# Performance work log

Measured on AMD Instinct MI355X. Metric: run time of the kernel, lower is better.

## Reference

```python
import jax, jax.numpy as jnp
import numpy as np

B, C, CI = 4, 1024, 512
T, H, W = 16, 28, 28
STD = 0.01  # init std used by the torch module
BN_EPS = 1e-5


def _conv1x1(x, w, b):
    # x: (B,C,T,H,W), w: (O,C), b: (O,)
    return jnp.einsum('bcthw,oc->bothw', x, w) + b[None, :, None, None, None]


def _maxpool2(x):
    # 3D max pool, kernel=stride=2 over (T,H,W)
    b, c, t, h, w = x.shape
    x = x.reshape(b, c, t // 2, 2, h // 2, 2, w // 2, 2)
    return x.max(axis=(3, 5, 7))


def setup_inputs() -> dict:
    key = jax.random.key(0)
    ks = jax.random.split(key, 6)
    return {
        'x': jax.random.normal(ks[0], (B, C, T, H, W), jnp.float32),
        'g_w': STD * jax.random.normal(ks[1], (CI, C), jnp.float32),
        'g_b': jnp.zeros((CI,), jnp.float32),
        'theta_w': STD * jax.random.normal(ks[2], (CI, C), jnp.float32),
        'theta_b': jnp.zeros((CI,), jnp.float32),
        'phi_w': STD * jax.random.normal(ks[3], (CI, C), jnp.float32),
        'phi_b': jnp.zeros((CI,), jnp.float32),
        'w_w': STD * jax.random.normal(ks[4], (C, CI), jnp.float32),
        'w_b': jnp.zeros((C,), jnp.float32),
        'bn_gamma': STD * jax.random.normal(ks[5], (C,), jnp.float32),
        'bn_beta': jnp.zeros((C,), jnp.float32),
    }


def reference(x, g_w, g_b, theta_w, theta_b, phi_w, phi_b, w_w, w_b, bn_gamma, bn_beta):
    b = x.shape[0]
    # g and phi branches are sub-sampled by maxpool(2)
    g_x = _maxpool2(_conv1x1(x, g_w, g_b)).reshape(b, CI, -1)          # (B,Ci,M)
    g_x = g_x.transpose(0, 2, 1)                                        # (B,M,Ci)
    theta_x = _conv1x1(x, theta_w, theta_b).reshape(b, CI, -1)          # (B,Ci,N)
    theta_x = theta_x.transpose(0, 2, 1)                                # (B,N,Ci)
    phi_x = _maxpool2(_conv1x1(x, phi_w, phi_b)).reshape(b, CI, -1)     # (B,Ci,M)
    # embedded gaussian: softmax(theta @ phi) @ g  (unscaled)
    f = jnp.einsum('bnc,bcm->bnm', theta_x, phi_x)                      # (B,N,M)
    f_div_C = jax.nn.softmax(f, axis=-1)
    y = jnp.einsum('bnm,bmc->bnc', f_div_C, g_x)                        # (B,N,Ci)
    y = y.transpose(0, 2, 1).reshape(b, CI, *x.shape[2:])               # (B,Ci,T,H,W)
    # W: 1x1 conv + BatchNorm (eval mode: running_mean=0, running_var=1)
    w_y = _conv1x1(y, w_w, w_b)
    scale = bn_gamma / jnp.sqrt(jnp.float32(1.0) + BN_EPS)
    w_y = w_y * scale[None, :, None, None, None] + bn_beta[None, :, None, None, None]
    return w_y + x
```

## Files before the change

kernel.cpp:

```cpp
#include <hip/hip_runtime.h>

#define DEVI __device__ __forceinline__

typedef __bf16 bf16x8 __attribute__((ext_vector_type(8)));
typedef float f32x4 __attribute__((ext_vector_type(4)));
typedef unsigned short u16;
typedef long long i64;

constexpr int B_ = 4;
constexpr int C_ = 1024;
constexpr int CI_ = 512;
constexpr int C3_ = 3 * CI_;
constexpr int N_ = 16 * 28 * 28;
constexpr int M_ = 8 * 14 * 14;
constexpr int MP_ = 1664;

DEVI u16 f2bf(float f) { __bf16 b = (__bf16)f; return __builtin_bit_cast(u16, b); }
DEVI float bf2f(u16 u) { return (float)__builtin_bit_cast(__bf16, u); }

#define GLOBAL_AS __attribute__((address_space(1)))
#define LDS_AS __attribute__((address_space(3)))

DEVI void load16(const u16* g, u16* l) {
  __builtin_amdgcn_global_load_lds((const GLOBAL_AS void*)g, (LDS_AS void*)l, 16, 0, 0);
}

template <int MODE>
__global__ __launch_bounds__(256)
void gemm_tn(const u16* __restrict__ A, const u16* __restrict__ Bm,
             void* __restrict__ Cp, int K, int lda, int ldb, int ldc,
             i64 sA, i64 sB, i64 sC,
             const float* __restrict__ e0, const float* __restrict__ e1,
             const float* __restrict__ e2, const float* __restrict__ xres, i64 sX) {
  __shared__ u16 lA[128 * 64];
  __shared__ u16 lB[128 * 64];
  const int b = blockIdx.z;
  A += (size_t)b * sA;
  Bm += (size_t)b * sB;
  const size_t cbase = (size_t)b * sC;
  xres += (MODE == 3) ? (size_t)b * sX : 0;

  const int tid = threadIdx.x;
  const int lane = tid & 63;
  const int wr = ((tid >> 6) >> 1) * 64;
  const int wc = ((tid >> 6) & 1) * 64;
  const int i0 = blockIdx.y * 128;
  const int j0 = blockIdx.x * 128;

  f32x4 acc[4][4] = {};

  const int srow = tid >> 3;
  const int scol = (tid & 7) * 8;
  const u16* Ag = A + (size_t)(i0 + srow) * lda + scol;
  const u16* Bg = Bm + (size_t)(j0 + srow) * ldb + scol;
  u16* lAw = lA + srow * 64 + scol;
  u16* lBw = lB + srow * 64 + scol;

  const int lrow = lane & 15;
  const int lq = (lane >> 4) * 8;

  for (int k0 = 0; k0 < K; k0 += 64) {
    __syncthreads();
#pragma unroll
    for (int q = 0; q < 4; ++q) load16(Ag + (size_t)q * 32 * lda + k0, lAw + q * 32 * 64);
#pragma unroll
    for (int q = 0; q < 4; ++q) load16(Bg + (size_t)q * 32 * ldb + k0, lBw + q * 32 * 64);
    __syncthreads();
#pragma unroll
    for (int ks = 0; ks < 2; ++ks) {
      bf16x8 af[4], bfr[4];
#pragma unroll
      for (int mi = 0; mi < 4; ++mi)
        af[mi] = *(const bf16x8*)&lA[(wr + mi * 16 + lrow) * 64 + ks * 32 + lq];
#pragma unroll
      for (int ni = 0; ni < 4; ++ni)
        bfr[ni] = *(const bf16x8*)&lB[(wc + ni * 16 + lrow) * 64 + ks * 32 + lq];
#pragma unroll
      for (int mi = 0; mi < 4; ++mi)
#pragma unroll
        for (int ni = 0; ni < 4; ++ni)
          acc[mi][ni] = __builtin_amdgcn_mfma_f32_16x16x32_bf16(af[mi], bfr[ni], acc[mi][ni], 0, 0, 0);
    }
  }

  const int r0 = i0 + wr + ((lane >> 4) << 2);
  const int c0 = j0 + wc + (lane & 15);
  float* Cf = (float*)Cp;
  u16* Cs = (u16*)Cp;
#pragma unroll
  for (int mi = 0; mi < 4; ++mi) {
#pragma unroll
    for (int ni = 0; ni < 4; ++ni) {
      const int col = c0 + ni * 16;
#pragma unroll
      for (int r = 0; r < 4; ++r) {
        const int row = r0 + mi * 16 + r;
        const size_t idx = cbase + (size_t)row * ldc + col;
        float v = acc[mi][ni][r];
        if constexpr (MODE == 0) {
          Cs[idx] = f2bf(v + e0[col]);
        } else if constexpr (MODE == 1) {
          Cs[idx] = f2bf(v);
        } else {
          const float sc = e1[row] * rsqrtf(1.0f + 1e-5f);
          Cf[idx] = (v + e0[row]) * sc + e2[row] + xres[(size_t)row * ldc + col];
        }
      }
    }
  }
}

__global__ __launch_bounds__(256)
void transpose_cast_x(const float* __restrict__ src, u16* __restrict__ dst) {
  __shared__ u16 tile[32][33];
  const size_t so = (size_t)blockIdx.z * C_ * N_;
  const int n0 = blockIdx.x * 32;
  const int c0 = blockIdx.y * 32;
  const int tx = threadIdx.x & 31;
  const int ty = threadIdx.x >> 5;
#pragma unroll
  for (int rr = 0; rr < 32; rr += 8)
    tile[ty + rr][tx] = f2bf(src[so + (size_t)(c0 + ty + rr) * N_ + n0 + tx]);
  __syncthreads();
#pragma unroll
  for (int rr = 0; rr < 32; rr += 8)
    dst[so + (size_t)(n0 + ty + rr) * C_ + c0 + tx] = tile[tx][ty + rr];
}

__global__ __launch_bounds__(256)
void transpose_bf16(const u16* __restrict__ src, u16* __restrict__ dst) {
  __shared__ u16 tile[32][33];
  const int b = blockIdx.z;
  const int c0 = blockIdx.x * 32;
  const int r0 = blockIdx.y * 32;
  const int tx = threadIdx.x & 31;
  const int ty = threadIdx.x >> 5;
#pragma unroll
  for (int rr = 0; rr < 32; rr += 8)
    tile[ty + rr][tx] = src[(size_t)b * MP_ * CI_ + (size_t)(r0 + ty + rr) * CI_ + c0 + tx];
  __syncthreads();
#pragma unroll
  for (int rr = 0; rr < 32; rr += 8)
    dst[(size_t)b * CI_ * MP_ + (size_t)(c0 + ty + rr) * MP_ + r0 + tx] = tile[tx][ty + rr];
}

__global__ __launch_bounds__(256)
void cast_weights(const float* s0, const float* s1, const float* s2, const float* s3,
                  u16* d0, u16* d1, u16* d2, u16* d3) {
  const int idx = blockIdx.x * 256 + threadIdx.x;
  const float* s;
  u16* d;
  switch (blockIdx.y) {
    case 0: s = s0; d = d0; break;
    case 1: s = s1; d = d1; break;
    case 2: s = s2; d = d2; break;
    default: s = s3; d = d3; break;
  }
  d[idx] = f2bf(s[idx]);
}

__global__ __launch_bounds__(256)
void concat_bias(const float* tb, const float* gb, const float* pb, float* dst) {
  const int i = blockIdx.x * 256 + threadIdx.x;
  if (i >= C3_) return;
  dst[i] = (i < CI_) ? tb[i] : (i < 2 * CI_) ? gb[i - CI_] : pb[i - 2 * CI_];
}

__global__ __launch_bounds__(256)
void pool2(const u16* __restrict__ CO, u16* __restrict__ Gp, u16* __restrict__ Pp) {
  const int b = blockIdx.z;
  const int which = blockIdx.y;
  const u16* src = CO + (size_t)b * N_ * C3_ + CI_ + which * CI_;
  u16* dst = (which ? Pp : Gp) + (size_t)b * MP_ * CI_;
  const int idx = blockIdx.x * 256 + threadIdx.x;
  const int m = idx >> 9;
  const int ci = idx & 511;
  if (m >= M_) { dst[idx] = 0; return; }
  const int t = m / 196, r = m % 196, h = r / 14, w = r % 14;
  const int nb = 2 * t * 784 + 2 * h * 28 + 2 * w;
  float mx = -1e30f;
#pragma unroll
  for (int dt = 0; dt < 2; ++dt)
#pragma unroll
    for (int dh = 0; dh < 2; ++dh)
#pragma unroll
      for (int dw = 0; dw < 2; ++dw)
        mx = fmaxf(mx, bf2f(src[(size_t)(nb + dt * 784 + dh * 28 + dw) * C3_ + ci]));
  dst[idx] = f2bf(mx);
}

__global__ __launch_bounds__(256)
void softmax_k(u16* __restrict__ F) {
  u16* row = F + ((size_t)blockIdx.y * N_ + blockIdx.x) * MP_;
  const int tid = threadIdx.x;
  float v[7];
  float mx = -1e30f;
#pragma unroll
  for (int it = 0; it < 7; ++it) {
    const int j = tid + it * 256;
    v[it] = (j < M_) ? bf2f(row[j]) : -1e30f;
    mx = fmaxf(mx, v[it]);
  }
#pragma unroll
  for (int off = 32; off >= 1; off >>= 1) mx = fmaxf(mx, __shfl_xor(mx, off));
  __shared__ float redm[4], reds[4];
  const int wv = tid >> 6;
  if ((tid & 63) == 0) redm[wv] = mx;
  __syncthreads();
  mx = fmaxf(fmaxf(redm[0], redm[1]), fmaxf(redm[2], redm[3]));
  float s = 0.f;
#pragma unroll
  for (int it = 0; it < 7; ++it) {
    const int j = tid + it * 256;
    v[it] = (j < M_) ? __expf(v[it] - mx) : 0.f;
    s += v[it];
  }
#pragma unroll
  for (int off = 32; off >= 1; off >>= 1) s += __shfl_xor(s, off);
  if ((tid & 63) == 0) reds[wv] = s;
  __syncthreads();
  s = reds[0] + reds[1] + reds[2] + reds[3];
  const float inv = 1.f / s;
#pragma unroll
  for (int it = 0; it < 7; ++it) {
    const int j = tid + it * 256;
    if (j < MP_) row[j] = f2bf(v[it] * inv);
  }
}

extern "C" void kernel_launch(void* const* d_in, const int* in_sizes, int n_in,
                              void* d_out, int out_size, void* d_ws, size_t ws_size,
                              hipStream_t stream) {
  (void)in_sizes; (void)n_in; (void)out_size;
  const float* x    = (const float*)d_in[0];
  const float* g_w  = (const float*)d_in[1];
  const float* g_b  = (const float*)d_in[2];
  const float* th_w = (const float*)d_in[3];
  const float* th_b = (const float*)d_in[4];
  const float* ph_w = (const float*)d_in[5];
  const float* ph_b = (const float*)d_in[6];
  const float* w_w  = (const float*)d_in[7];
  const float* w_b  = (const float*)d_in[8];
  const float* bn_g = (const float*)d_in[9];
  const float* bn_b = (const float*)d_in[10];
  float* out = (float*)d_out;

  auto align256 = [](size_t b) { return (b + 255) & ~(size_t)255; };
  const size_t fixed_bytes = align256((size_t)C3_ * C_ * 2) + align256((size_t)C_ * CI_ * 2) +
                             align256((size_t)C3_ * 4);
  const size_t per_batch = align256((size_t)N_ * C_ * 2)
                         + align256((size_t)N_ * C3_ * 2)
                         + align256((size_t)N_ * MP_ * 2)
                         + align256((size_t)N_ * CI_ * 2)
                         + 3 * align256((size_t)MP_ * CI_ * 2);
  int G = 4;
  while (G > 1 && fixed_bytes + (size_t)G * per_batch > ws_size) G >>= 1;

  char* ws = (char*)d_ws;
  size_t off = 0;
  auto alloc = [&](size_t bytes) -> void* {
    void* p = ws + off;
    off += align256(bytes);
    return p;
  };
  u16* wcat = (u16*)alloc((size_t)C3_ * C_ * 2);
  u16* wwB  = (u16*)alloc((size_t)C_ * CI_ * 2);
  float* eb = (float*)alloc((size_t)C3_ * 4);
  u16* Xt  = (u16*)alloc((size_t)G * N_ * C_ * 2);
  u16* CO  = (u16*)alloc((size_t)G * N_ * C3_ * 2);
  u16* Fb  = (u16*)alloc((size_t)G * N_ * MP_ * 2);
  u16* Yb  = (u16*)alloc((size_t)G * N_ * CI_ * 2);
  u16* Gp  = (u16*)alloc((size_t)G * MP_ * CI_ * 2);
  u16* Pp  = (u16*)alloc((size_t)G * MP_ * CI_ * 2);
  u16* Gp2 = (u16*)alloc((size_t)G * CI_ * MP_ * 2);

  const dim3 blk(256);
  cast_weights<<<dim3(2048, 4), blk, 0, stream>>>(
      th_w, g_w, ph_w, w_w, wcat, wcat + (size_t)CI_ * C_, wcat + (size_t)2 * CI_ * C_, wwB);
  concat_bias<<<dim3(6), blk, 0, stream>>>(th_b, g_b, ph_b, eb);

  for (int bg = 0; bg < B_; bg += G) {
    const float* xg = x + (size_t)bg * C_ * N_;
    float* og = out + (size_t)bg * C_ * N_;
    transpose_cast_x<<<dim3(N_ / 32, C_ / 32, G), blk, 0, stream>>>(xg, Xt);
    gemm_tn<0><<<dim3(C3_ / 128, G * N_ / 128, 1), blk, 0, stream>>>(
        Xt, wcat, CO, C_, C_, C_, C3_, 0, 0, 0, eb, nullptr, nullptr, nullptr, 0);
    pool2<<<dim3(MP_ * CI_ / 256, 2, G), blk, 0, stream>>>(CO, Gp, Pp);
    transpose_bf16<<<dim3(CI_ / 32, MP_ / 32, G), blk, 0, stream>>>(Gp, Gp2);
    gemm_tn<1><<<dim3(MP_ / 128, N_ / 128, G), blk, 0, stream>>>(
        CO, Pp, Fb, CI_, C3_, CI_, MP_,
        (i64)N_ * C3_, (i64)MP_ * CI_, (i64)N_ * MP_, nullptr, nullptr, nullptr, nullptr, 0);
    softmax_k<<<dim3(N_, G), blk, 0, stream>>>(Fb);
    gemm_tn<1><<<dim3(CI_ / 128, N_ / 128, G), blk, 0, stream>>>(
        Fb, Gp2, Yb, MP_, MP_, MP_, CI_,
        (i64)N_ * MP_, (i64)CI_ * MP_, (i64)N_ * CI_, nullptr, nullptr, nullptr, nullptr, 0);
    gemm_tn<3><<<dim3(N_ / 128, C_ / 128, G), blk, 0, stream>>>(
        wwB, Yb, og, CI_, CI_, CI_, N_,
        0, (i64)N_ * CI_, (i64)C_ * N_, w_b, bn_g, bn_b, xg, (i64)C_ * N_);
  }
}
```

Measured before the change: 1.192 ms.

## Rewrite GEMM as 256x256 tile, 512-thread double-buffered pipelined kernel with swizzled LDS

Replaces the single-buffered 128x128 GEMM with a 256x256 tile computed by 8 waves, double-buffered LDS staging split into K halves, manual vmcnt waits, and an XOR swizzle to avoid LDS bank conflicts. MP is padded to 1792 so the M dimension divides by 256. The aim is to overlap global loads with MFMA work and raise data reuse per tile. In exchange, every GEMM now launches far fewer blocks, which may hurt occupancy on the small GEMMs, and the padded M increases softmax and GEMM work.

```diff
diff --git a/kernel.cpp b/kernel.cpp
--- a/kernel.cpp
+++ b/kernel.cpp
@@ -13,7 +13,7 @@
 constexpr int C3_ = 3 * CI_;
 constexpr int N_ = 16 * 28 * 28;
 constexpr int M_ = 8 * 14 * 14;
-constexpr int MP_ = 1664;
+constexpr int MP_ = 1792;
 
 DEVI u16 f2bf(float f) { __bf16 b = (__bf16)f; return __builtin_bit_cast(u16, b); }
 DEVI float bf2f(u16 u) { return (float)__builtin_bit_cast(__bf16, u); }
@@ -25,76 +25,126 @@
   __builtin_amdgcn_global_load_lds((const GLOBAL_AS void*)g, (LDS_AS void*)l, 16, 0, 0);
 }
 
+#define SYNC_V(N)                                        \
+  asm volatile("s_waitcnt vmcnt(" #N ")" ::: "memory");  \
+  __builtin_amdgcn_s_barrier();                          \
+  asm volatile("" ::: "memory");
+
 template <int MODE>
-__global__ __launch_bounds__(256)
+__global__ __launch_bounds__(512, 2)
 void gemm_tn(const u16* __restrict__ A, const u16* __restrict__ Bm,
              void* __restrict__ Cp, int K, int lda, int ldb, int ldc,
              i64 sA, i64 sB, i64 sC,
              const float* __restrict__ e0, const float* __restrict__ e1,
              const float* __restrict__ e2, const float* __restrict__ xres, i64 sX) {
-  __shared__ u16 lA[128 * 64];
-  __shared__ u16 lB[128 * 64];
+  __shared__ u16 sm[2 * 32768];
   const int b = blockIdx.z;
   A += (size_t)b * sA;
   Bm += (size_t)b * sB;
   const size_t cbase = (size_t)b * sC;
-  xres += (MODE == 3) ? (size_t)b * sX : 0;
+  if constexpr (MODE == 3) xres += (size_t)b * sX;
 
   const int tid = threadIdx.x;
   const int lane = tid & 63;
-  const int wr = ((tid >> 6) >> 1) * 64;
-  const int wc = ((tid >> 6) & 1) * 64;
-  const int i0 = blockIdx.y * 128;
-  const int j0 = blockIdx.x * 128;
-
-  f32x4 acc[4][4] = {};
-
-  const int srow = tid >> 3;
-  const int scol = (tid & 7) * 8;
-  const u16* Ag = A + (size_t)(i0 + srow) * lda + scol;
-  const u16* Bg = Bm + (size_t)(j0 + srow) * ldb + scol;
-  u16* lAw = lA + srow * 64 + scol;
-  u16* lBw = lB + srow * 64 + scol;
-
-  const int lrow = lane & 15;
-  const int lq = (lane >> 4) * 8;
-
-  for (int k0 = 0; k0 < K; k0 += 64) {
-    __syncthreads();
-#pragma unroll
-    for (int q = 0; q < 4; ++q) load16(Ag + (size_t)q * 32 * lda + k0, lAw + q * 32 * 64);
-#pragma unroll
-    for (int q = 0; q < 4; ++q) load16(Bg + (size_t)q * 32 * ldb + k0, lBw + q * 32 * 64);
-    __syncthreads();
-#pragma unroll
-    for (int ks = 0; ks < 2; ++ks) {
-      bf16x8 af[4], bfr[4];
-#pragma unroll
-      for (int mi = 0; mi < 4; ++mi)
-        af[mi] = *(const bf16x8*)&lA[(wr + mi * 16 + lrow) * 64 + ks * 32 + lq];
-#pragma unroll
-      for (int ni = 0; ni < 4; ++ni)
-        bfr[ni] = *(const bf16x8*)&lB[(wc + ni * 16 + lrow) * 64 + ks * 32 + lq];
-#pragma unroll
-      for (int mi = 0; mi < 4; ++mi)
-#pragma unroll
-        for (int ni = 0; ni < 4; ++ni)
-          acc[mi][ni] = __builtin_amdgcn_mfma_f32_16x16x32_bf16(af[mi], bfr[ni], acc[mi][ni], 0, 0, 0);
-    }
-  }
-
-  const int r0 = i0 + wr + ((lane >> 4) << 2);
-  const int c0 = j0 + wc + (lane & 15);
+  const int wave = tid >> 6;
+  const int wm = wave >> 2;
+  const int wn = wave & 3;
+  const int i0 = blockIdx.y * 256;
+  const int j0 = blockIdx.x * 256;
+
+  const int rs = tid >> 2;
+  const int swz = ((tid & 3) ^ ((rs >> 1) & 3)) * 8;
+  const u16* Ag0 = A + (size_t)(i0 + rs) * lda + swz;
+  const u16* Bg0 = Bm + (size_t)(j0 + rs) * ldb + swz;
+  const i64 ldA128 = (i64)128 * lda;
+  const i64 ldB128 = (i64)128 * ldb;
+  u16* ldsT = sm + tid * 8;
+
+  auto stA = [&](int buf, int kh, int k0) {
+    const u16* s = Ag0 + k0 + kh * 32;
+    u16* d = ldsT + buf * 32768 + kh * 8192;
+    load16(s, d);
+    load16(s + ldA128, d + 4096);
+  };
+  auto stB = [&](int buf, int kh, int k0) {
+    const u16* s = Bg0 + k0 + kh * 32;
+    u16* d = ldsT + buf * 32768 + 16384 + kh * 8192;
+    load16(s, d);
+    load16(s + ldB128, d + 4096);
+  };
+
+  const int l15 = lane & 15;
+  const int slR = (((lane >> 4) ^ ((l15 >> 1) & 3)) * 8);
+  const int arow = wm * 128 + l15;
+  const int brow = wn * 64 + l15;
+
+  f32x4 acc[8][4] = {};
+
+#define KHALF(BUF, KH, S1, S2, SYNC)                                           \
+  {                                                                            \
+    const u16* Ab_ = sm + (BUF) * 32768 + (KH) * 8192;                         \
+    const u16* Bb_ = Ab_ + 16384;                                              \
+    bf16x8 bv[4], a0[4], a1[4];                                                \
+    _Pragma("unroll") for (int n = 0; n < 4; ++n)                              \
+        bv[n] = *(const bf16x8*)&Bb_[(brow + n * 16) * 32 + slR];              \
+    _Pragma("unroll") for (int f = 0; f < 4; ++f)                              \
+        a0[f] = *(const bf16x8*)&Ab_[(arow + f * 16) * 32 + slR];              \
+    S1;                                                                        \
+    __builtin_amdgcn_s_setprio(1);                                             \
+    _Pragma("unroll") for (int f = 0; f < 4; ++f)                              \
+        _Pragma("unroll") for (int n = 0; n < 4; ++n)                          \
+            acc[f][n] = __builtin_amdgcn_mfma_f32_16x16x32_bf16(               \
+                a0[f], bv[n], acc[f][n], 0, 0, 0);                             \
+    __builtin_amdgcn_s_setprio(0);                                             \
+    _Pragma("unroll") for (int f = 0; f < 4; ++f)                              \
+        a1[f] = *(const bf16x8*)&Ab_[(arow + (f + 4) * 16) * 32 + slR];        \
+    S2;                                                                        \
+    __builtin_amdgcn_s_setprio(1);                                             \
+    _Pragma("unroll") for (int f = 0; f < 4; ++f)                              \
+        _Pragma("unroll") for (int n = 0; n < 4; ++n)                          \
+            acc[f + 4][n] = __builtin_amdgcn_mfma_f32_16x16x32_bf16(           \
+                a1[f], bv[n], acc[f + 4][n], 0, 0, 0);                         \
+    __builtin_amdgcn_s_setprio(0);                                             \
+    SYNC                                                                       \
+  }
+
+  const int NT = K >> 6;
+
+  stA(0, 0, 0); stB(0, 0, 0);
+  stA(0, 1, 0); stB(0, 1, 0);
+  stA(1, 0, 64); stB(1, 0, 64);
+  SYNC_V(8);
+
+  for (int t = 0; t < NT - 2; ++t) {
+    const int bc = t & 1;
+    const int k0 = t * 64;
+    KHALF(bc, 0, stA(bc ^ 1, 1, k0 + 64), stB(bc ^ 1, 1, k0 + 64), SYNC_V(8));
+    KHALF(bc, 1, stA(bc, 0, k0 + 128), stB(bc, 0, k0 + 128), SYNC_V(8));
+  }
+  {
+    const int bc = (NT - 2) & 1;
+    stA(bc ^ 1, 1, (NT - 1) * 64);
+    stB(bc ^ 1, 1, (NT - 1) * 64);
+    SYNC_V(0);
+    KHALF(bc, 0, (void)0, (void)0, );
+    KHALF(bc, 1, (void)0, (void)0, );
+    KHALF(bc ^ 1, 0, (void)0, (void)0, );
+    KHALF(bc ^ 1, 1, (void)0, (void)0, );
+  }
+#undef KHALF
+
+  const int rr0 = i0 + wm * 128 + ((lane >> 4) << 2);
+  const int cc0 = j0 + wn * 64 + (lane & 15);
   float* Cf = (float*)Cp;
   u16* Cs = (u16*)Cp;
 #pragma unroll
-  for (int mi = 0; mi < 4; ++mi) {
+  for (int mi = 0; mi < 8; ++mi) {
 #pragma unroll
     for (int ni = 0; ni < 4; ++ni) {
-      const int col = c0 + ni * 16;
+      const int col = cc0 + ni * 16;
 #pragma unroll
       for (int r = 0; r < 4; ++r) {
-        const int row = r0 + mi * 16 + r;
+        const int row = rr0 + mi * 16 + r;
         const size_t idx = cbase + (size_t)row * ldc + col;
         float v = acc[mi][ni][r];
         if constexpr (MODE == 0) {
@@ -275,6 +325,7 @@
   u16* Gp2 = (u16*)alloc((size_t)G * CI_ * MP_ * 2);
 
   const dim3 blk(256);
+  const dim3 gblk(512);
   cast_weights<<<dim3(2048, 4), blk, 0, stream>>>(
       th_w, g_w, ph_w, w_w, wcat, wcat + (size_t)CI_ * C_, wcat + (size_t)2 * CI_ * C_, wwB);
   concat_bias<<<dim3(6), blk, 0, stream>>>(th_b, g_b, ph_b, eb);
@@ -283,18 +334,18 @@
     const float* xg = x + (size_t)bg * C_ * N_;
     float* og = out + (size_t)bg * C_ * N_;
     transpose_cast_x<<<dim3(N_ / 32, C_ / 32, G), blk, 0, stream>>>(xg, Xt);
-    gemm_tn<0><<<dim3(C3_ / 128, G * N_ / 128, 1), blk, 0, stream>>>(
+    gemm_tn<0><<<dim3(C3_ / 256, G * N_ / 256, 1), gblk, 0, stream>>>(
         Xt, wcat, CO, C_, C_, C_, C3_, 0, 0, 0, eb, nullptr, nullptr, nullptr, 0);
     pool2<<<dim3(MP_ * CI_ / 256, 2, G), blk, 0, stream>>>(CO, Gp, Pp);
     transpose_bf16<<<dim3(CI_ / 32, MP_ / 32, G), blk, 0, stream>>>(Gp, Gp2);
-    gemm_tn<1><<<dim3(MP_ / 128, N_ / 128, G), blk, 0, stream>>>(
+    gemm_tn<1><<<dim3(MP_ / 256, N_ / 256, G), gblk, 0, stream>>>(
         CO, Pp, Fb, CI_, C3_, CI_, MP_,
         (i64)N_ * C3_, (i64)MP_ * CI_, (i64)N_ * MP_, nullptr, nullptr, nullptr, nullptr, 0);
     softmax_k<<<dim3(N_, G), blk, 0, stream>>>(Fb);
-    gemm_tn<1><<<dim3(CI_ / 128, N_ / 128, G), blk, 0, stream>>>(
+    gemm_tn<1><<<dim3(CI_ / 256, N_ / 256, G), gblk, 0, stream>>>(
         Fb, Gp2, Yb, MP_, MP_, MP_, CI_,
         (i64)N_ * MP_, (i64)CI_ * MP_, (i64)N_ * CI_, nullptr, nullptr, nullptr, nullptr, 0);
-    gemm_tn<3><<<dim3(N_ / 128, C_ / 128, G), blk, 0, stream>>>(
+    gemm_tn<3><<<dim3(N_ / 256, C_ / 256, G), gblk, 0, stream>>>(
         wwB, Yb, og, CI_, CI_, CI_, N_,
         0, (i64)N_ * CI_, (i64)C_ * N_, w_b, bn_g, bn_b, xg, (i64)C_ * N_);
   }
```

Result: faster. 1.014 ms (-14.9%).
